# Kernel tuning notes

Measured on AMD Instinct MI355X. Metric: run time of the kernel, lower is better.

The kernel has to match this reference:

```python
import jax, jax.numpy as jnp
import numpy as np

S = 4096      # total packed tokens
DIM = 1280    # hidden dim
H = 16        # num heads
HD = DIM // H # head dim = 80


def setup_inputs() -> dict:
    key = jax.random.key(0)
    ks = jax.random.split(key, 5)
    hidden_states = jax.random.normal(ks[0], (S, DIM), jnp.float32)
    # realistic rotary tables: [S, HD] with duplicated half-frequencies
    inv_freq = 1.0 / (10000.0 ** (np.arange(0, HD // 2, dtype=np.float64) / (HD // 2)))
    ang = np.arange(S, dtype=np.float64)[:, None] * inv_freq[None, :]          # [S, HD/2]
    emb = np.concatenate([ang, ang], axis=-1)                                   # [S, HD]
    cos = jnp.asarray(np.cos(emb), jnp.float32)
    sin = jnp.asarray(np.sin(emb), jnp.float32)
    scale = 1.0 / np.sqrt(DIM)
    qkv_w = jax.random.normal(ks[1], (3 * DIM, DIM), jnp.float32) * scale
    qkv_b = jax.random.normal(ks[2], (3 * DIM,), jnp.float32) * 0.02
    proj_w = jax.random.normal(ks[3], (DIM, DIM), jnp.float32) * scale
    proj_b = jax.random.normal(ks[4], (DIM,), jnp.float32) * 0.02
    # ragged segment boundaries: must start at 0 and end at S
    cu_seqlens = jnp.asarray([0, 300, 900, 1500, 2300, 2900, 3500, 4000, 4096], jnp.int32)
    return {
        "hidden_states": hidden_states,
        "cos": cos,
        "sin": sin,
        "qkv_w": qkv_w,
        "qkv_b": qkv_b,
        "proj_w": proj_w,
        "proj_b": proj_b,
        "cu_seqlens": cu_seqlens,
    }


def _rotate_half(x):
    x1, x2 = jnp.split(x, 2, axis=-1)
    return jnp.concatenate([-x2, x1], axis=-1)


def reference(hidden_states, cos, sin, qkv_w, qkv_b, proj_w, proj_b, cu_seqlens):
    seq_len, dim = hidden_states.shape
    hd = dim // H
    qkv = (hidden_states @ qkv_w.T + qkv_b).reshape(seq_len, 3, H, hd)
    q, k, v = qkv[:, 0], qkv[:, 1], qkv[:, 2]                 # each [S, H, hd]
    # RoPE in float32, broadcast cos/sin over heads
    c = cos[:, None, :].astype(jnp.float32)
    s = sin[:, None, :].astype(jnp.float32)
    qf = q.astype(jnp.float32)
    kf = k.astype(jnp.float32)
    q = (qf * c + _rotate_half(qf) * s).astype(q.dtype)
    k = (kf * c + _rotate_half(kf) * s).astype(k.dtype)
    # block-diagonal additive mask: segment id per token
    pos = jnp.arange(seq_len)
    seg = jnp.searchsorted(cu_seqlens[1:], pos, side='right')  # [S]
    neg = jnp.finfo(jnp.float32).min
    bias = jnp.where(seg[:, None] == seg[None, :], 0.0, neg)   # [S, S]
    attn = jnp.einsum('shd,thd->hst', q, k) / np.sqrt(hd) + bias[None]
    w = jax.nn.softmax(attn.astype(jnp.float32), axis=-1).astype(q.dtype)
    out = jnp.einsum('hst,thd->shd', w, v).reshape(seq_len, dim)
    return out @ proj_w.T + proj_b
```

## Files before the change

### kernel.cpp

```cpp
#include <hip/hip_runtime.h>
#include <hip/hip_bf16.h>
#include <stdint.h>

#define SQ 4096
#define DM 1280
#define NH 16
#define HDIM 80
#define N_QKV 3840

typedef __attribute__((ext_vector_type(8))) short short8;
typedef __attribute__((ext_vector_type(4))) float f32x4;

__device__ __forceinline__ unsigned short f2bf(float f) {
  union { float f; unsigned int u; } v; v.f = f;
  unsigned int r = v.u + 0x7FFFu + ((v.u >> 16) & 1u);
  return (unsigned short)(r >> 16);
}
__device__ __forceinline__ float bf2f(unsigned short u) {
  union { unsigned int u; float f; } v; v.u = ((unsigned int)u) << 16;
  return v.f;
}

__global__ __launch_bounds__(256) void cvt_all(const float* __restrict__ hidden,
                                               const float* __restrict__ qkv_w,
                                               const float* __restrict__ proj_w,
                                               unsigned short* __restrict__ oh,
                                               unsigned short* __restrict__ oq,
                                               unsigned short* __restrict__ op) {
  int b = blockIdx.x;
  const float* in;
  unsigned short* out;
  int base;
  if (b < 5120) { in = hidden; out = oh; base = b; }
  else if (b < 9920) { in = qkv_w; out = oq; base = b - 5120; }
  else { in = proj_w; out = op; base = b - 9920; }
  int i = base * 256 + threadIdx.x;
  float4 v = reinterpret_cast<const float4*>(in)[i];
  ushort4 o;
  o.x = f2bf(v.x); o.y = f2bf(v.y); o.z = f2bf(v.z); o.w = f2bf(v.w);
  reinterpret_cast<ushort4*>(out)[i] = o;
}

__device__ __forceinline__ void gload_lds16(const void* g, void* l) {
  __builtin_amdgcn_global_load_lds(
      (const __attribute__((address_space(1))) void*)g,
      (__attribute__((address_space(3))) void*)l, 16, 0, 0);
}

template <int OUT_BF16>
__global__ __launch_bounds__(256, 3) void gemm_bt(const unsigned short* __restrict__ A,
                                                  const unsigned short* __restrict__ B,
                                                  const float* __restrict__ bias,
                                                  void* __restrict__ C, int M, int N, int K,
                                                  int nbx) {
  __shared__ __align__(16) unsigned short As[3][128 * 32];
  __shared__ __align__(16) unsigned short Bs[3][128 * 32];
  const int tid = threadIdx.x;
  const int wave = tid >> 6, lane = tid & 63;
  const int r15 = lane & 15, kg = lane >> 4;
  const int wr = wave >> 1, wc = wave & 1;

  const int b = blockIdx.x;
  const int c = b & 7, i = b >> 3;
  const int by = (c & 3) * 8 + (i & 7);
  const int bx = (c >> 2) * (nbx >> 1) + (i >> 3);
  const int tm = by * 128, tn = bx * 128;

  f32x4 acc[4][4];
#pragma unroll
  for (int x = 0; x < 4; ++x)
#pragma unroll
    for (int j = 0; j < 4; ++j) acc[x][j] = {0.f, 0.f, 0.f, 0.f};

  const int slot0 = wave * 64 + lane;
  const int row0 = slot0 >> 2, k80 = (slot0 & 3) << 3;
  const int slot1 = slot0 + 256;
  const int row1 = slot1 >> 2, k81 = (slot1 & 3) << 3;
  const unsigned short* Arow0 = A + (size_t)(tm + row0) * K + k80;
  const unsigned short* Arow1 = A + (size_t)(tm + row1) * K + k81;
  const unsigned short* Brow0 = B + (size_t)(tn + row0) * K + k80;
  const unsigned short* Brow1 = B + (size_t)(tn + row1) * K + k81;
  const int ldsoff0 = (wave * 64) * 8;
  const int ldsoff1 = (wave * 64 + 256) * 8;

  auto stage = [&](int kt, int buf) {
    gload_lds16(Arow0 + kt, &As[buf][ldsoff0]);
    gload_lds16(Arow1 + kt, &As[buf][ldsoff1]);
    gload_lds16(Brow0 + kt, &Bs[buf][ldsoff0]);
    gload_lds16(Brow1 + kt, &Bs[buf][ldsoff1]);
  };

  const int nk = K >> 5;
  stage(0, 0);
  if (nk > 1) stage(32, 1);

  int buf = 0;
  for (int t = 0; t < nk; ++t) {
    if (t + 2 < nk) {
      stage((t + 2) << 5, (buf + 2) % 3);
      asm volatile("s_waitcnt vmcnt(8)" ::: "memory");
    } else if (t + 1 < nk) {
      asm volatile("s_waitcnt vmcnt(4)" ::: "memory");
    } else {
      asm volatile("s_waitcnt vmcnt(0)" ::: "memory");
    }
    __builtin_amdgcn_sched_barrier(0);
    __builtin_amdgcn_s_barrier();

    short8 af[4], bfr[4];
#pragma unroll
    for (int mi = 0; mi < 4; ++mi)
      af[mi] = *reinterpret_cast<const short8*>(&As[buf][(wr * 64 + mi * 16 + r15) * 32 + kg * 8]);
#pragma unroll
    for (int ni = 0; ni < 4; ++ni)
      bfr[ni] = *reinterpret_cast<const short8*>(&Bs[buf][(wc * 64 + ni * 16 + r15) * 32 + kg * 8]);
    __builtin_amdgcn_s_setprio(1);
#pragma unroll
    for (int mi = 0; mi < 4; ++mi)
#pragma unroll
      for (int ni = 0; ni < 4; ++ni)
        acc[mi][ni] = __builtin_amdgcn_mfma_f32_16x16x32_bf16(af[mi], bfr[ni], acc[mi][ni], 0, 0, 0);
    __builtin_amdgcn_s_setprio(0);

    __builtin_amdgcn_s_barrier();
    __builtin_amdgcn_sched_barrier(0);
    buf = (buf + 1) % 3;
  }

#pragma unroll
  for (int mi = 0; mi < 4; ++mi) {
#pragma unroll
    for (int ni = 0; ni < 4; ++ni) {
      int col = tn + wc * 64 + ni * 16 + r15;
      float bv = bias[col];
#pragma unroll
      for (int r = 0; r < 4; ++r) {
        int row = tm + wr * 64 + mi * 16 + kg * 4 + r;
        float v = acc[mi][ni][r] + bv;
        if (OUT_BF16)
          ((unsigned short*)C)[(size_t)row * N + col] = f2bf(v);
        else
          ((float*)C)[(size_t)row * N + col] = v;
      }
    }
  }
}

__global__ __launch_bounds__(256) void rope_v_kernel(unsigned short* __restrict__ qkv,
                                                     const float* __restrict__ cosb,
                                                     const float* __restrict__ sinb,
                                                     unsigned short* __restrict__ Vt) {
  const float SC = 0.1118033988749895f;
  int h = blockIdx.y, s0 = blockIdx.x * 64;
  __shared__ unsigned short vt[64][80];
  for (int e = threadIdx.x; e < 64 * 40; e += 256) {
    int sl = e / 40, dp = e % 40;
    int s = s0 + sl;
    float c = cosb[s * HDIM + dp];
    float sn = sinb[s * HDIM + dp];
    size_t qb = (size_t)s * N_QKV + h * HDIM;
    float q1 = bf2f(qkv[qb + dp]), q2 = bf2f(qkv[qb + dp + 40]);
    qkv[qb + dp] = f2bf((q1 * c - q2 * sn) * SC);
    qkv[qb + dp + 40] = f2bf((q2 * c + q1 * sn) * SC);
    size_t kb = qb + DM;
    float k1 = bf2f(qkv[kb + dp]), k2 = bf2f(qkv[kb + dp + 40]);
    qkv[kb + dp] = f2bf(k1 * c - k2 * sn);
    qkv[kb + dp + 40] = f2bf(k2 * c + k1 * sn);
    size_t vb = qb + 2 * DM;
    vt[sl][dp] = qkv[vb + dp];
    vt[sl][dp + 40] = qkv[vb + dp + 40];
  }
  __syncthreads();
  for (int e = threadIdx.x; e < HDIM * 64; e += 256) {
    int d = e >> 6, sl = e & 63;
    Vt[((size_t)h * HDIM + d) * SQ + s0 + sl] = vt[sl][d];
  }
}

template <int CTRL>
__device__ __forceinline__ float dpp_f(float x) {
  int xi = __builtin_bit_cast(int, x);
  int r = __builtin_amdgcn_update_dpp(xi, xi, CTRL, 0xf, 0xf, true);
  return __builtin_bit_cast(float, r);
}
__device__ __forceinline__ float rowmax16(float x) {
  x = fmaxf(x, dpp_f<0xB1>(x));
  x = fmaxf(x, dpp_f<0x4E>(x));
  x = fmaxf(x, dpp_f<0x141>(x));
  x = fmaxf(x, dpp_f<0x140>(x));
  return x;
}
__device__ __forceinline__ float rowsum16(float x) {
  x += dpp_f<0xB1>(x);
  x += dpp_f<0x4E>(x);
  x += dpp_f<0x141>(x);
  x += dpp_f<0x140>(x);
  return x;
}

__global__ __launch_bounds__(256, 2) void attn_kernel(const unsigned short* __restrict__ qkv,
                                                      const unsigned short* __restrict__ Vt,
                                                      const int* __restrict__ cu, int nseg,
                                                      unsigned short* __restrict__ attn_out) {
  constexpr int PROW = 68;
  __shared__ __align__(16) unsigned char Kl[2][64 * 256];
  __shared__ __align__(16) unsigned char Vl[2][80 * 128];
  __shared__ __align__(16) unsigned short Pl[4][16 * PROW];
  __shared__ int cus[32];

  const int tid = threadIdx.x;
  const int wave = tid >> 6, lane = tid & 63;
  const int r15 = lane & 15, kg = lane >> 4;
  const int s7 = r15 & 7;
  const short8 z8 = {0, 0, 0, 0, 0, 0, 0, 0};

  const int b = blockIdx.x;
  const int xcd = b & 7, j = b >> 3;
  const int h = xcd * 2 + (j >> 6);
  const int qt = j & 63;

  if (tid <= nseg) cus[tid] = cu[tid];
  __syncthreads();

  auto seg_of = [&](int pos) {
    int s2 = 0;
    for (int i2 = 1; i2 < nseg; ++i2)
      if (pos >= cus[i2]) s2 = i2;
    return s2;
  };

  const int tbase = qt * 64;
  const int wbase = tbase + wave * 16;
  int rs[4], re[4];
#pragma unroll
  for (int r = 0; r < 4; ++r) {
    int sg = seg_of(wbase + kg * 4 + r);
    rs[r] = cus[sg];
    re[r] = cus[sg + 1];
  }
  const int seg_lo = seg_of(wbase), seg_hi = seg_of(wbase + 15);
  const int w_lo = cus[seg_lo], w_hi = cus[seg_hi + 1];
  const int rs_hi = cus[seg_hi], re_lo = cus[seg_lo + 1];

  const int kb0 = cus[seg_of(tbase)] & ~63;
  const int kend = cus[seg_of(tbase + 63) + 1];
  const int nt = (kend - kb0 + 63) >> 6;

  const unsigned short* qp = qkv + (size_t)(wbase + r15) * N_QKV + h * HDIM;
  short8 qf[3];
#pragma unroll
  for (int ds = 0; ds < 3; ++ds) {
    int d0 = ds * 32 + kg * 8;
    qf[ds] = (d0 < HDIM) ? *reinterpret_cast<const short8*>(qp + d0) : z8;
  }

  float m[4] = {-1e30f, -1e30f, -1e30f, -1e30f};
  float l[4] = {0.f, 0.f, 0.f, 0.f};
  f32x4 acc[5];
#pragma unroll
  for (int dg = 0; dg < 5; ++dg) acc[dg] = {0.f, 0.f, 0.f, 0.f};

  const unsigned short* kbase = qkv + DM + (size_t)h * HDIM;
  const unsigned short* vbase = Vt + (size_t)h * HDIM * SQ;
  unsigned short* pw = &Pl[wave][0];
  const int wub = tid & ~63;

  auto issue_stage = [&](int kb, int buf) {
    unsigned char* kd = &Kl[buf][0];
    unsigned char* vd = &Vl[buf][0];
#pragma unroll
    for (int p = 0; p < 4; ++p) {
      int L = p * 256 + tid;
      int row = L >> 4;
      int c = (L & 15) ^ (row & 7);
      int csrc = (c < 10) ? c : 0;
      gload_lds16(kbase + (size_t)(kb + row) * N_QKV + csrc * 8,
                  kd + (p * 256 + wub) * 16);
    }
#pragma unroll
    for (int p = 0; p < 2; ++p) {
      int L = p * 256 + tid;
      int row = L >> 3;
      int c = (L & 7) ^ (row & 7);
      gload_lds16(vbase + (size_t)row * SQ + kb + c * 8,
                  vd + (p * 256 + wub) * 16);
    }
    {
      int L = 512 + (wub >> 1) + (lane & 31);
      int row = L >> 3;
      int c = (L & 7) ^ (row & 7);
      if (lane < 32)
        gload_lds16(vbase + (size_t)row * SQ + kb + c * 8,
                    vd + (512 + (wub >> 1)) * 16);
    }
  };

  issue_stage(kb0, 0);
  int cur = 0;

  for (int t = 0; t < nt; ++t) {
    const int k0 = kb0 + (t << 6);
    if (t + 1 < nt) {
      issue_stage(k0 + 64, cur ^ 1);
      asm volatile("s_waitcnt vmcnt(7)" ::: "memory");
    } else {
      asm volatile("s_waitcnt vmcnt(0)" ::: "memory");
    }
    __builtin_amdgcn_sched_barrier(0);
    __builtin_amdgcn_s_barrier();

    const bool active = (k0 < w_hi) && (k0 + 64 > w_lo);
    if (active) {
      const unsigned char* Kc = &Kl[cur][0];
      const unsigned char* Vc = &Vl[cur][0];

      f32x4 sa[4];
#pragma unroll
      for (int g = 0; g < 4; ++g) sa[g] = {0.f, 0.f, 0.f, 0.f};
#pragma unroll
      for (int g = 0; g < 4; ++g) {
        const unsigned char* kr = Kc + ((g * 16 + r15) << 8);
#pragma unroll
        for (int ds = 0; ds < 3; ++ds) {
          int d0 = ds * 32 + kg * 8;
          short8 kf = (d0 < HDIM)
              ? *reinterpret_cast<const short8*>(kr + (((ds * 4 + kg) ^ s7) << 4))
              : z8;
          sa[g] = __builtin_amdgcn_mfma_f32_16x16x32_bf16(qf[ds], kf, sa[g], 0, 0, 0);
        }
      }

      short8 vf[5][2];
#pragma unroll
      for (int dg = 0; dg < 5; ++dg)
#pragma unroll
        for (int g2 = 0; g2 < 2; ++g2)
          vf[dg][g2] = *reinterpret_cast<const short8*>(
              Vc + ((dg * 16 + r15) << 7) + (((g2 * 4 + kg) ^ s7) << 4));

      const bool interior = (k0 >= rs_hi) && (k0 + 64 <= re_lo);
      float corr[4];
      bool resc;
      if (interior) {
        float mx4[4];
#pragma unroll
        for (int r = 0; r < 4; ++r)
          mx4[r] = rowmax16(fmaxf(fmaxf(sa[0][r], sa[1][r]), fmaxf(sa[2][r], sa[3][r])));
        int defer = (mx4[0] <= m[0] + 8.f) && (mx4[1] <= m[1] + 8.f) &&
                    (mx4[2] <= m[2] + 8.f) && (mx4[3] <= m[3] + 8.f);
        if (__all(defer)) {
          resc = false;
#pragma unroll
          for (int r = 0; r < 4; ++r) {
            unsigned short* prow = pw + (kg * 4 + r) * PROW;
            float sm = 0.f;
#pragma unroll
            for (int g = 0; g < 4; ++g) {
              float pv = __expf(sa[g][r] - m[r]);
              sm += pv;
              prow[g * 16 + r15] = f2bf(pv);
            }
            l[r] += rowsum16(sm);
          }
        } else {
          resc = true;
#pragma unroll
          for (int r = 0; r < 4; ++r) {
            unsigned short* prow = pw + (kg * 4 + r) * PROW;
            float mn = fmaxf(m[r], mx4[r]);
            corr[r] = __expf(m[r] - mn);
            float sm = 0.f;
#pragma unroll
            for (int g = 0; g < 4; ++g) {
              float pv = __expf(sa[g][r] - mn);
              sm += pv;
              prow[g * 16 + r15] = f2bf(pv);
            }
            l[r] = l[r] * corr[r] + rowsum16(sm);
            m[r] = mn;
          }
        }
      } else {
        resc = true;
#pragma unroll
        for (int r = 0; r < 4; ++r) {
          unsigned short* prow = pw + (kg * 4 + r) * PROW;
          float vv[4];
#pragma unroll
          for (int g = 0; g < 4; ++g) {
            int key = k0 + g * 16 + r15;
            vv[g] = (key >= rs[r] && key < re[r]) ? sa[g][r] : -1e30f;
          }
          float mx = rowmax16(fmaxf(fmaxf(vv[0], vv[1]), fmaxf(vv[2], vv[3])));
          float mn = fmaxf(m[r], mx);
          corr[r] = __expf(m[r] - mn);
          float sm = 0.f;
#pragma unroll
          for (int g = 0; g < 4; ++g) {
            float pv = __expf(vv[g] - mn);
            sm += pv;
            prow[g * 16 + r15] = f2bf(pv);
          }
          l[r] = l[r] * corr[r] + rowsum16(sm);
          m[r] = mn;
        }
      }
      if (resc) {
#pragma unroll
        for (int dg = 0; dg < 5; ++dg) {
          f32x4 t2 = acc[dg];
          t2[0] *= corr[0]; t2[1] *= corr[1]; t2[2] *= corr[2]; t2[3] *= corr[3];
          acc[dg] = t2;
        }
      }

      asm volatile("s_waitcnt lgkmcnt(0)" ::: "memory");
      __builtin_amdgcn_sched_barrier(0);
      const unsigned short* prd = pw + r15 * PROW;
      union { short8 v; uint2 d[2]; } pu[2];
#pragma unroll
      for (int g2 = 0; g2 < 2; ++g2) {
        pu[g2].d[0] = *reinterpret_cast<const uint2*>(prd + g2 * 32 + kg * 8);
        pu[g2].d[1] = *reinterpret_cast<const uint2*>(prd + g2 * 32 + kg * 8 + 4);
      }

      __builtin_amdgcn_s_setprio(1);
#pragma unroll
      for (int dg = 0; dg < 5; ++dg)
#pragma unroll
        for (int g2 = 0; g2 < 2; ++g2)
          acc[dg] = __builtin_amdgcn_mfma_f32_16x16x32_bf16(pu[g2].v, vf[dg][g2], acc[dg], 0, 0, 0);
      __builtin_amdgcn_s_setprio(0);
    }

    __builtin_amdgcn_s_barrier();
    cur ^= 1;
  }

#pragma unroll
  for (int r = 0; r < 4; ++r) {
    int row = wbase + kg * 4 + r;
    float inv = 1.0f / l[r];
#pragma unroll
    for (int dg = 0; dg < 5; ++dg)
      attn_out[(size_t)row * DM + h * HDIM + dg * 16 + r15] = f2bf(acc[dg][r] * inv);
  }
}

extern "C" void kernel_launch(void* const* d_in, const int* in_sizes, int n_in,
                              void* d_out, int out_size, void* d_ws, size_t ws_size,
                              hipStream_t stream) {
  const float* hidden = (const float*)d_in[0];
  const float* cosb = (const float*)d_in[1];
  const float* sinb = (const float*)d_in[2];
  const float* qkv_w = (const float*)d_in[3];
  const float* qkv_b = (const float*)d_in[4];
  const float* proj_w = (const float*)d_in[5];
  const float* proj_b = (const float*)d_in[6];
  const int* cu = (const int*)d_in[7];
  int nseg = in_sizes[7] - 1;
  float* out = (float*)d_out;

  char* ws = (char*)d_ws;
  unsigned short* Ah = (unsigned short*)(ws);
  unsigned short* Wq = (unsigned short*)(ws + 10485760);
  unsigned short* Wp = (unsigned short*)(ws + 10485760 + 9830400);
  unsigned short* qkvB = (unsigned short*)(ws + 23592960);
  unsigned short* Vt = (unsigned short*)(ws + 23592960 + 31457280);
  unsigned short* attn_out = Ah;

  cvt_all<<<dim3(11520), dim3(256), 0, stream>>>(hidden, qkv_w, proj_w, Ah, Wq, Wp);
  gemm_bt<1><<<dim3(960), dim3(256), 0, stream>>>(Ah, Wq, qkv_b, qkvB, SQ, N_QKV, DM, 30);
  rope_v_kernel<<<dim3(64, NH), dim3(256), 0, stream>>>(qkvB, cosb, sinb, Vt);
  attn_kernel<<<dim3(1024), dim3(256), 0, stream>>>(qkvB, Vt, cu, nseg, attn_out);
  gemm_bt<0><<<dim3(320), dim3(256), 0, stream>>>(attn_out, Wp, proj_b, out, SQ, DM, DM, 10);
}
```

Before: 193.1 us.

## Process 32 query rows per wave to reuse K/V tiles across two row groups

```diff
diff --git a/kernel.cpp b/kernel.cpp
--- a/kernel.cpp
+++ b/kernel.cpp
@@ -205,7 +205,7 @@
   constexpr int PROW = 68;
   __shared__ __align__(16) unsigned char Kl[2][64 * 256];
   __shared__ __align__(16) unsigned char Vl[2][80 * 128];
-  __shared__ __align__(16) unsigned short Pl[4][16 * PROW];
+  __shared__ __align__(16) unsigned short Pl[4][32 * PROW];
   __shared__ int cus[32];
 
   const int tid = threadIdx.x;
@@ -216,8 +216,8 @@
 
   const int b = blockIdx.x;
   const int xcd = b & 7, j = b >> 3;
-  const int h = xcd * 2 + (j >> 6);
-  const int qt = j & 63;
+  const int h = xcd * 2 + (j >> 5);
+  const int qt = j & 31;
 
   if (tid <= nseg) cus[tid] = cu[tid];
   __syncthreads();
@@ -229,36 +229,45 @@
     return s2;
   };
 
-  const int tbase = qt * 64;
-  const int wbase = tbase + wave * 16;
-  int rs[4], re[4];
-#pragma unroll
-  for (int r = 0; r < 4; ++r) {
-    int sg = seg_of(wbase + kg * 4 + r);
-    rs[r] = cus[sg];
-    re[r] = cus[sg + 1];
-  }
-  const int seg_lo = seg_of(wbase), seg_hi = seg_of(wbase + 15);
+  const int tbase = qt * 128;
+  const int wbase = tbase + wave * 32;
+  int rs[2][4], re[2][4];
+#pragma unroll
+  for (int rg = 0; rg < 2; ++rg)
+#pragma unroll
+    for (int r = 0; r < 4; ++r) {
+      int sg = seg_of(wbase + rg * 16 + kg * 4 + r);
+      rs[rg][r] = cus[sg];
+      re[rg][r] = cus[sg + 1];
+    }
+  const int seg_lo = seg_of(wbase), seg_hi = seg_of(wbase + 31);
   const int w_lo = cus[seg_lo], w_hi = cus[seg_hi + 1];
   const int rs_hi = cus[seg_hi], re_lo = cus[seg_lo + 1];
 
   const int kb0 = cus[seg_of(tbase)] & ~63;
-  const int kend = cus[seg_of(tbase + 63) + 1];
+  const int kend = cus[seg_of(tbase + 127) + 1];
   const int nt = (kend - kb0 + 63) >> 6;
 
-  const unsigned short* qp = qkv + (size_t)(wbase + r15) * N_QKV + h * HDIM;
-  short8 qf[3];
-#pragma unroll
-  for (int ds = 0; ds < 3; ++ds) {
-    int d0 = ds * 32 + kg * 8;
-    qf[ds] = (d0 < HDIM) ? *reinterpret_cast<const short8*>(qp + d0) : z8;
-  }
-
-  float m[4] = {-1e30f, -1e30f, -1e30f, -1e30f};
-  float l[4] = {0.f, 0.f, 0.f, 0.f};
-  f32x4 acc[5];
-#pragma unroll
-  for (int dg = 0; dg < 5; ++dg) acc[dg] = {0.f, 0.f, 0.f, 0.f};
+  short8 qf[2][3];
+#pragma unroll
+  for (int rg = 0; rg < 2; ++rg) {
+    const unsigned short* qp = qkv + (size_t)(wbase + rg * 16 + r15) * N_QKV + h * HDIM;
+#pragma unroll
+    for (int ds = 0; ds < 3; ++ds) {
+      int d0 = ds * 32 + kg * 8;
+      qf[rg][ds] = (d0 < HDIM) ? *reinterpret_cast<const short8*>(qp + d0) : z8;
+    }
+  }
+
+  float m[2][4], l[2][4];
+  f32x4 acc[2][5];
+#pragma unroll
+  for (int rg = 0; rg < 2; ++rg) {
+#pragma unroll
+    for (int r = 0; r < 4; ++r) { m[rg][r] = -1e30f; l[rg][r] = 0.f; }
+#pragma unroll
+    for (int dg = 0; dg < 5; ++dg) acc[rg][dg] = {0.f, 0.f, 0.f, 0.f};
+  }
 
   const unsigned short* kbase = qkv + DM + (size_t)h * HDIM;
   const unsigned short* vbase = Vt + (size_t)h * HDIM * SQ;
@@ -314,9 +323,11 @@
       const unsigned char* Kc = &Kl[cur][0];
       const unsigned char* Vc = &Vl[cur][0];
 
-      f32x4 sa[4];
-#pragma unroll
-      for (int g = 0; g < 4; ++g) sa[g] = {0.f, 0.f, 0.f, 0.f};
+      f32x4 sa[2][4];
+#pragma unroll
+      for (int rg = 0; rg < 2; ++rg)
+#pragma unroll
+        for (int g = 0; g < 4; ++g) sa[rg][g] = {0.f, 0.f, 0.f, 0.f};
 #pragma unroll
       for (int g = 0; g < 4; ++g) {
         const unsigned char* kr = Kc + ((g * 16 + r15) << 8);
@@ -326,7 +337,8 @@
           short8 kf = (d0 < HDIM)
               ? *reinterpret_cast<const short8*>(kr + (((ds * 4 + kg) ^ s7) << 4))
               : z8;
-          sa[g] = __builtin_amdgcn_mfma_f32_16x16x32_bf16(qf[ds], kf, sa[g], 0, 0, 0);
+          sa[0][g] = __builtin_amdgcn_mfma_f32_16x16x32_bf16(qf[0][ds], kf, sa[0][g], 0, 0, 0);
+          sa[1][g] = __builtin_amdgcn_mfma_f32_16x16x32_bf16(qf[1][ds], kf, sa[1][g], 0, 0, 0);
         }
       }
 
@@ -339,97 +351,117 @@
               Vc + ((dg * 16 + r15) << 7) + (((g2 * 4 + kg) ^ s7) << 4));
 
       const bool interior = (k0 >= rs_hi) && (k0 + 64 <= re_lo);
-      float corr[4];
+      float corr[2][4];
       bool resc;
       if (interior) {
-        float mx4[4];
-#pragma unroll
-        for (int r = 0; r < 4; ++r)
-          mx4[r] = rowmax16(fmaxf(fmaxf(sa[0][r], sa[1][r]), fmaxf(sa[2][r], sa[3][r])));
-        int defer = (mx4[0] <= m[0] + 8.f) && (mx4[1] <= m[1] + 8.f) &&
-                    (mx4[2] <= m[2] + 8.f) && (mx4[3] <= m[3] + 8.f);
+        float mx4[2][4];
+#pragma unroll
+        for (int rg = 0; rg < 2; ++rg)
+#pragma unroll
+          for (int r = 0; r < 4; ++r)
+            mx4[rg][r] = rowmax16(fmaxf(fmaxf(sa[rg][0][r], sa[rg][1][r]),
+                                        fmaxf(sa[rg][2][r], sa[rg][3][r])));
+        int defer = 1;
+#pragma unroll
+        for (int rg = 0; rg < 2; ++rg)
+#pragma unroll
+          for (int r = 0; r < 4; ++r) defer &= (mx4[rg][r] <= m[rg][r] + 8.f);
         if (__all(defer)) {
           resc = false;
 #pragma unroll
+          for (int rg = 0; rg < 2; ++rg)
+#pragma unroll
+            for (int r = 0; r < 4; ++r) {
+              unsigned short* prow = pw + (rg * 16 + kg * 4 + r) * PROW;
+              float sm = 0.f;
+#pragma unroll
+              for (int g = 0; g < 4; ++g) {
+                float pv = __expf(sa[rg][g][r] - m[rg][r]);
+                sm += pv;
+                prow[g * 16 + r15] = f2bf(pv);
+              }
+              l[rg][r] += rowsum16(sm);
+            }
+        } else {
+          resc = true;
+#pragma unroll
+          for (int rg = 0; rg < 2; ++rg)
+#pragma unroll
+            for (int r = 0; r < 4; ++r) {
+              unsigned short* prow = pw + (rg * 16 + kg * 4 + r) * PROW;
+              float mn = fmaxf(m[rg][r], mx4[rg][r]);
+              corr[rg][r] = __expf(m[rg][r] - mn);
+              float sm = 0.f;
+#pragma unroll
+              for (int g = 0; g < 4; ++g) {
+                float pv = __expf(sa[rg][g][r] - mn);
+                sm += pv;
+                prow[g * 16 + r15] = f2bf(pv);
+              }
+              l[rg][r] = l[rg][r] * corr[rg][r] + rowsum16(sm);
+              m[rg][r] = mn;
+            }
+        }
+      } else {
+        resc = true;
+#pragma unroll
+        for (int rg = 0; rg < 2; ++rg)
+#pragma unroll
           for (int r = 0; r < 4; ++r) {
-            unsigned short* prow = pw + (kg * 4 + r) * PROW;
+            unsigned short* prow = pw + (rg * 16 + kg * 4 + r) * PROW;
+            float vv[4];
+#pragma unroll
+            for (int g = 0; g < 4; ++g) {
+              int key = k0 + g * 16 + r15;
+              vv[g] = (key >= rs[rg][r] && key < re[rg][r]) ? sa[rg][g][r] : -1e30f;
+            }
+            float mx = rowmax16(fmaxf(fmaxf(vv[0], vv[1]), fmaxf(vv[2], vv[3])));
+            float mn = fmaxf(m[rg][r], mx);
+            corr[rg][r] = __expf(m[rg][r] - mn);
             float sm = 0.f;
 #pragma unroll
             for (int g = 0; g < 4; ++g) {
-              float pv = __expf(sa[g][r] - m[r]);
+              float pv = __expf(vv[g] - mn);
               sm += pv;
               prow[g * 16 + r15] = f2bf(pv);
             }
-            l[r] += rowsum16(sm);
+            l[rg][r] = l[rg][r] * corr[rg][r] + rowsum16(sm);
+            m[rg][r] = mn;
           }
-        } else {
-          resc = true;
-#pragma unroll
-          for (int r = 0; r < 4; ++r) {
-            unsigned short* prow = pw + (kg * 4 + r) * PROW;
-            float mn = fmaxf(m[r], mx4[r]);
-            corr[r] = __expf(m[r] - mn);
-            float sm = 0.f;
-#pragma unroll
-            for (int g = 0; g < 4; ++g) {
-              float pv = __expf(sa[g][r] - mn);
-              sm += pv;
-              prow[g * 16 + r15] = f2bf(pv);
-            }
-            l[r] = l[r] * corr[r] + rowsum16(sm);
-            m[r] = mn;
+      }
+      if (resc) {
+#pragma unroll
+        for (int rg = 0; rg < 2; ++rg)
+#pragma unroll
+          for (int dg = 0; dg < 5; ++dg) {
+            f32x4 t2 = acc[rg][dg];
+            t2[0] *= corr[rg][0]; t2[1] *= corr[rg][1];
+            t2[2] *= corr[rg][2]; t2[3] *= corr[rg][3];
+            acc[rg][dg] = t2;
           }
-        }
-      } else {
-        resc = true;
-#pragma unroll
-        for (int r = 0; r < 4; ++r) {
-          unsigned short* prow = pw + (kg * 4 + r) * PROW;
-          float vv[4];
-#pragma unroll
-          for (int g = 0; g < 4; ++g) {
-            int key = k0 + g * 16 + r15;
-            vv[g] = (key >= rs[r] && key < re[r]) ? sa[g][r] : -1e30f;
-          }
-          float mx = rowmax16(fmaxf(fmaxf(vv[0], vv[1]), fmaxf(vv[2], vv[3])));
-          float mn = fmaxf(m[r], mx);
-          corr[r] = __expf(m[r] - mn);
-          float sm = 0.f;
-#pragma unroll
-          for (int g = 0; g < 4; ++g) {
-            float pv = __expf(vv[g] - mn);
-            sm += pv;
-            prow[g * 16 + r15] = f2bf(pv);
-          }
-          l[r] = l[r] * corr[r] + rowsum16(sm);
-          m[r] = mn;
+      }
+
+      asm volatile("s_waitcnt lgkmcnt(0)" ::: "memory");
+      __builtin_amdgcn_sched_barrier(0);
+      union { short8 v; uint2 d[2]; } pu[2][2];
+#pragma unroll
+      for (int rg = 0; rg < 2; ++rg) {
+        const unsigned short* prd = pw + (rg * 16 + r15) * PROW;
+#pragma unroll
+        for (int g2 = 0; g2 < 2; ++g2) {
+          pu[rg][g2].d[0] = *reinterpret_cast<const uint2*>(prd + g2 * 32 + kg * 8);
+          pu[rg][g2].d[1] = *reinterpret_cast<const uint2*>(prd + g2 * 32 + kg * 8 + 4);
         }
       }
-      if (resc) {
-#pragma unroll
-        for (int dg = 0; dg < 5; ++dg) {
-          f32x4 t2 = acc[dg];
-          t2[0] *= corr[0]; t2[1] *= corr[1]; t2[2] *= corr[2]; t2[3] *= corr[3];
-          acc[dg] = t2;
+
+      __builtin_amdgcn_s_setprio(1);
+#pragma unroll
+      for (int dg = 0; dg < 5; ++dg)
+#pragma unroll
+        for (int g2 = 0; g2 < 2; ++g2) {
+          acc[0][dg] = __builtin_amdgcn_mfma_f32_16x16x32_bf16(pu[0][g2].v, vf[dg][g2], acc[0][dg], 0, 0, 0);
+          acc[1][dg] = __builtin_amdgcn_mfma_f32_16x16x32_bf16(pu[1][g2].v, vf[dg][g2], acc[1][dg], 0, 0, 0);
         }
-      }
-
-      asm volatile("s_waitcnt lgkmcnt(0)" ::: "memory");
-      __builtin_amdgcn_sched_barrier(0);
-      const unsigned short* prd = pw + r15 * PROW;
-      union { short8 v; uint2 d[2]; } pu[2];
-#pragma unroll
-      for (int g2 = 0; g2 < 2; ++g2) {
-        pu[g2].d[0] = *reinterpret_cast<const uint2*>(prd + g2 * 32 + kg * 8);
-        pu[g2].d[1] = *reinterpret_cast<const uint2*>(prd + g2 * 32 + kg * 8 + 4);
-      }
-
-      __builtin_amdgcn_s_setprio(1);
-#pragma unroll
-      for (int dg = 0; dg < 5; ++dg)
-#pragma unroll
-        for (int g2 = 0; g2 < 2; ++g2)
-          acc[dg] = __builtin_amdgcn_mfma_f32_16x16x32_bf16(pu[g2].v, vf[dg][g2], acc[dg], 0, 0, 0);
       __builtin_amdgcn_s_setprio(0);
     }
 
@@ -438,13 +470,15 @@
   }
 
 #pragma unroll
-  for (int r = 0; r < 4; ++r) {
-    int row = wbase + kg * 4 + r;
-    float inv = 1.0f / l[r];
-#pragma unroll
-    for (int dg = 0; dg < 5; ++dg)
-      attn_out[(size_t)row * DM + h * HDIM + dg * 16 + r15] = f2bf(acc[dg][r] * inv);
-  }
+  for (int rg = 0; rg < 2; ++rg)
+#pragma unroll
+    for (int r = 0; r < 4; ++r) {
+      int row = wbase + rg * 16 + kg * 4 + r;
+      float inv = 1.0f / l[rg][r];
+#pragma unroll
+      for (int dg = 0; dg < 5; ++dg)
+        attn_out[(size_t)row * DM + h * HDIM + dg * 16 + r15] = f2bf(acc[rg][dg][r] * inv);
+    }
 }
 
 extern "C" void kernel_launch(void* const* d_in, const int* in_sizes, int n_in,
@@ -472,6 +506,6 @@
   cvt_all<<<dim3(11520), dim3(256), 0, stream>>>(hidden, qkv_w, proj_w, Ah, Wq, Wp);
   gemm_bt<1><<<dim3(960), dim3(256), 0, stream>>>(Ah, Wq, qkv_b, qkvB, SQ, N_QKV, DM, 30);
   rope_v_kernel<<<dim3(64, NH), dim3(256), 0, stream>>>(qkvB, cosb, sinb, Vt);
-  attn_kernel<<<dim3(1024), dim3(256), 0, stream>>>(qkvB, Vt, cu, nseg, attn_out);
+  attn_kernel<<<dim3(512), dim3(256), 0, stream>>>(qkvB, Vt, cu, nseg, attn_out);
   gemm_bt<0><<<dim3(320), dim3(256), 0, stream>>>(attn_out, Wp, proj_b, out, SQ, DM, DM, 10);
 }
```

New measurement: 229.6 us. 1.19x slower.

## Use 256x128 GEMM tiles with 512-thread blocks sharing B tile

Applied to the files above, without the earlier changes.

```diff
diff --git a/kernel.cpp b/kernel.cpp
--- a/kernel.cpp
+++ b/kernel.cpp
@@ -48,12 +48,12 @@
 }
 
 template <int OUT_BF16>
-__global__ __launch_bounds__(256, 3) void gemm_bt(const unsigned short* __restrict__ A,
-                                                  const unsigned short* __restrict__ B,
-                                                  const float* __restrict__ bias,
-                                                  void* __restrict__ C, int M, int N, int K,
-                                                  int nbx) {
-  __shared__ __align__(16) unsigned short As[3][128 * 32];
+__global__ __launch_bounds__(512, 4) void gemm_bt2(const unsigned short* __restrict__ A,
+                                                   const unsigned short* __restrict__ B,
+                                                   const float* __restrict__ bias,
+                                                   void* __restrict__ C, int M, int N, int K,
+                                                   int nbx) {
+  __shared__ __align__(16) unsigned short As[3][256 * 32];
   __shared__ __align__(16) unsigned short Bs[3][128 * 32];
   const int tid = threadIdx.x;
   const int wave = tid >> 6, lane = tid & 63;
@@ -62,9 +62,9 @@
 
   const int b = blockIdx.x;
   const int c = b & 7, i = b >> 3;
-  const int by = (c & 3) * 8 + (i & 7);
-  const int bx = (c >> 2) * (nbx >> 1) + (i >> 3);
-  const int tm = by * 128, tn = bx * 128;
+  const int by = (c & 3) * 4 + (i & 3);
+  const int bx = (c >> 2) * (nbx >> 1) + (i >> 2);
+  const int tm = by * 256, tn = bx * 128;
 
   f32x4 acc[4][4];
 #pragma unroll
@@ -72,35 +72,29 @@
 #pragma unroll
     for (int j = 0; j < 4; ++j) acc[x][j] = {0.f, 0.f, 0.f, 0.f};
 
-  const int slot0 = wave * 64 + lane;
-  const int row0 = slot0 >> 2, k80 = (slot0 & 3) << 3;
-  const int slot1 = slot0 + 256;
-  const int row1 = slot1 >> 2, k81 = (slot1 & 3) << 3;
-  const unsigned short* Arow0 = A + (size_t)(tm + row0) * K + k80;
-  const unsigned short* Arow1 = A + (size_t)(tm + row1) * K + k81;
-  const unsigned short* Brow0 = B + (size_t)(tn + row0) * K + k80;
-  const unsigned short* Brow1 = B + (size_t)(tn + row1) * K + k81;
-  const int ldsoff0 = (wave * 64) * 8;
-  const int ldsoff1 = (wave * 64 + 256) * 8;
+  const int rowt = tid >> 2, k8t = (tid & 3) << 3;
+  const unsigned short* Arow0 = A + (size_t)(tm + rowt) * K + k8t;
+  const unsigned short* Arow1 = Arow0 + (size_t)128 * K;
+  const unsigned short* Brow = B + (size_t)(tn + rowt) * K + k8t;
+  const int ldsA0 = tid * 8, ldsA1 = (512 + tid) * 8, ldsB = tid * 8;
 
   auto stage = [&](int kt, int buf) {
-    gload_lds16(Arow0 + kt, &As[buf][ldsoff0]);
-    gload_lds16(Arow1 + kt, &As[buf][ldsoff1]);
-    gload_lds16(Brow0 + kt, &Bs[buf][ldsoff0]);
-    gload_lds16(Brow1 + kt, &Bs[buf][ldsoff1]);
+    gload_lds16(Arow0 + kt, &As[buf][ldsA0]);
+    gload_lds16(Arow1 + kt, &As[buf][ldsA1]);
+    gload_lds16(Brow + kt, &Bs[buf][ldsB]);
   };
 
   const int nk = K >> 5;
   stage(0, 0);
-  if (nk > 1) stage(32, 1);
+  stage(32, 1);
 
   int buf = 0;
   for (int t = 0; t < nk; ++t) {
     if (t + 2 < nk) {
       stage((t + 2) << 5, (buf + 2) % 3);
-      asm volatile("s_waitcnt vmcnt(8)" ::: "memory");
+      asm volatile("s_waitcnt vmcnt(6)" ::: "memory");
     } else if (t + 1 < nk) {
-      asm volatile("s_waitcnt vmcnt(4)" ::: "memory");
+      asm volatile("s_waitcnt vmcnt(3)" ::: "memory");
     } else {
       asm volatile("s_waitcnt vmcnt(0)" ::: "memory");
     }
@@ -470,8 +464,8 @@
   unsigned short* attn_out = Ah;
 
   cvt_all<<<dim3(11520), dim3(256), 0, stream>>>(hidden, qkv_w, proj_w, Ah, Wq, Wp);
-  gemm_bt<1><<<dim3(960), dim3(256), 0, stream>>>(Ah, Wq, qkv_b, qkvB, SQ, N_QKV, DM, 30);
+  gemm_bt2<1><<<dim3(480), dim3(512), 0, stream>>>(Ah, Wq, qkv_b, qkvB, SQ, N_QKV, DM, 30);
   rope_v_kernel<<<dim3(64, NH), dim3(256), 0, stream>>>(qkvB, cosb, sinb, Vt);
   attn_kernel<<<dim3(1024), dim3(256), 0, stream>>>(qkvB, Vt, cu, nseg, attn_out);
-  gemm_bt<0><<<dim3(320), dim3(256), 0, stream>>>(attn_out, Wp, proj_b, out, SQ, DM, DM, 10);
-}
+  gemm_bt2<0><<<dim3(160), dim3(512), 0, stream>>>(attn_out, Wp, proj_b, out, SQ, DM, DM, 10);
+}
```

Result: faster. 178.3 us (-7.7%).
